# Kernel optimization log

Hardware: AMD Instinct MI355X
Metric: run time of the kernel (lower is better)

Reference implementation:

```python
import jax, jax.numpy as jnp
import numpy as np

P, B, FEAT, HID, ATTN, NHEAD = 4096, 32, 512, 512, 512, 8
HD = ATTN // NHEAD  # 64


def setup_inputs() -> dict:
    key = jax.random.key(0)
    ks = jax.random.split(key, 12)
    s = lambda n: 1.0 / np.sqrt(n)
    return {
        "last_hidden": jax.random.normal(ks[0], (1, B, HID), jnp.float32),
        "encoder_outputs": jax.random.normal(ks[1], (P, B, FEAT), jnp.float32),
        # outer projections (stored [in, out]; torch Linear is x @ W.T + b)
        "Wa_w": jax.random.uniform(ks[2], (FEAT, ATTN), jnp.float32, -s(FEAT), s(FEAT)),
        "Wa_b": jax.random.uniform(ks[3], (ATTN,), jnp.float32, -s(FEAT), s(FEAT)),
        "Ua_w": jax.random.uniform(ks[4], (HID, ATTN), jnp.float32, -s(HID), s(HID)),
        "Ua_b": jax.random.uniform(ks[5], (ATTN,), jnp.float32, -s(HID), s(HID)),
        # inner Attention(head_attn_size, head_attn_size, head_attn_size)
        "Wa2_w": jax.random.uniform(ks[6], (HD, HD), jnp.float32, -s(HD), s(HD)),
        "Wa2_b": jax.random.uniform(ks[7], (HD,), jnp.float32, -s(HD), s(HD)),
        "Ua2_w": jax.random.uniform(ks[8], (HD, HD), jnp.float32, -s(HD), s(HD)),
        "Ua2_b": jax.random.uniform(ks[9], (HD,), jnp.float32, -s(HD), s(HD)),
        "va_w": jax.random.uniform(ks[10], (HD, 1), jnp.float32, -s(HD), s(HD)),
        "va_b": jax.random.uniform(ks[11], (1,), jnp.float32, -s(HD), s(HD)),
        "nhead": NHEAD,
    }


def reference(last_hidden, encoder_outputs, Wa_w, Wa_b, Ua_w, Ua_b,
              Wa2_w, Wa2_b, Ua2_w, Ua2_b, va_w, va_b, nhead):
    p, b = encoder_outputs.shape[:2]
    enc = encoder_outputs @ Wa_w + Wa_b            # [P,B,A]
    hid = last_hidden @ Ua_w + Ua_b                # [1,B,A]
    hd = enc.shape[-1] // nhead
    enc = enc.reshape(p, b, nhead, hd)             # [P,B,nh,hd]
    hid = hid.reshape(1, b, nhead, hd)             # [1,B,nh,hd]
    # inner Bahdanau attention
    a = jnp.tanh((enc @ Wa2_w + Wa2_b) + (hid @ Ua2_w + Ua2_b))
    scores = a @ va_w + va_b                       # [P,B,nh,1]
    weights = jax.nn.softmax(scores, axis=0)       # softmax over pixels
    context = jnp.sum(weights * enc, axis=0, keepdims=True)  # [1,B,nh,hd]
    weight = jnp.mean(weights, axis=-2)            # mean over heads -> [P,B,1]
    context = context.reshape(1, b, nhead * hd)    # [1,B,A]
    return context, weight
```

## Files before the change

kernel.cpp:

```cpp
#include <hip/hip_runtime.h>
#include <hip/hip_bf16.h>

#define PDIM 4096
#define BDIM 32
#define MDIM (PDIM*BDIM)
#define KDIM 512
#define NDIM 512
#define NH   8
#define HD   64

typedef __attribute__((ext_vector_type(4))) float f32x4;
typedef __attribute__((ext_vector_type(8))) short bf16x8;

__device__ __forceinline__ unsigned short f2bf(float f) {
  unsigned u = __float_as_uint(f);
  u += 0x7fffu + ((u >> 16) & 1u);
  return (unsigned short)(u >> 16);
}
__device__ __forceinline__ float bf2f(unsigned short u) {
  return __uint_as_float(((unsigned)u) << 16);
}

__device__ __forceinline__ float fast_tanh(float x) {
  x = fminf(fmaxf(x, -15.f), 15.f);
  float e = __expf(2.f * x);
  return __fdividef(e - 1.f, e + 1.f);
}

#define GLOAD_LDS16(g, l) __builtin_amdgcn_global_load_lds( \
    (const __attribute__((address_space(1))) void*)(g),     \
    (__attribute__((address_space(3))) void*)(l), 16, 0, 0)

__global__ __launch_bounds__(256) void cvt_k(
    const float* __restrict__ x, unsigned short* __restrict__ xbf) {
  size_t i = ((size_t)blockIdx.x * 256 + threadIdx.x) * 8;
  float4 a = *(const float4*)(x + i);
  float4 b = *(const float4*)(x + i + 4);
  ushort4 o0; o0.x = f2bf(a.x); o0.y = f2bf(a.y); o0.z = f2bf(a.z); o0.w = f2bf(a.w);
  ushort4 o1; o1.x = f2bf(b.x); o1.y = f2bf(b.y); o1.z = f2bf(b.z); o1.w = f2bf(b.w);
  *(ushort4*)(xbf + i) = o0;
  *(ushort4*)(xbf + i + 4) = o1;
}

__global__ __launch_bounds__(512) void hub_k(
    const float* __restrict__ lh, const float* __restrict__ Ua,
    const float* __restrict__ Ua_b, const float* __restrict__ Ua2,
    const float* __restrict__ Ua2_b, const float* __restrict__ Wa_b,
    const float* __restrict__ Wa2, const float* __restrict__ Wa2_b,
    float* __restrict__ ubf) {
  int b = blockIdx.x, tid = threadIdx.x;
  __shared__ float ls[512];
  __shared__ float hs[512];
  ls[tid] = lh[b*512 + tid];
  __syncthreads();
  float s = Ua_b[tid];
  #pragma unroll 8
  for (int k = 0; k < 512; ++k)
    s += ls[k] * Ua[(size_t)k*512 + tid];
  hs[tid] = s;
  __syncthreads();
  int h = tid >> 6, j = tid & 63;
  float u = Ua2_b[j] + Wa2_b[j];
  #pragma unroll 4
  for (int k = 0; k < 64; ++k) {
    u += hs[h*64 + k] * Ua2[k*64 + j];
    u += Wa_b[h*64 + k] * Wa2[k*64 + j];
  }
  ubf[b*512 + tid] = u;
}

__global__ __launch_bounds__(256) void wft_k(
    const float* __restrict__ Wa, const float* __restrict__ Wa2,
    unsigned short* __restrict__ WfT) {
  int n = blockIdx.x, tid = threadIdx.x;
  int h = n >> 6, j = n & 63;
  __shared__ float w2[64];
  if (tid < 64) w2[tid] = Wa2[tid*64 + j];
  __syncthreads();
  for (int k = tid; k < 512; k += 256) {
    float s = 0.f;
    #pragma unroll 8
    for (int kk = 0; kk < 64; ++kk)
      s += Wa[(size_t)k*512 + h*64 + kk] * w2[kk];
    WfT[(size_t)n*512 + k] = f2bf(s);
  }
}

__global__ __launch_bounds__(256, 3) void gemm_score_k(
    const unsigned short* __restrict__ xbf, const unsigned short* __restrict__ WfT,
    const float* __restrict__ ubf, const float* __restrict__ va_w,
    const float* __restrict__ va_b, float* __restrict__ scores) {
  __shared__ __align__(16) unsigned short As[8192];
  __shared__ __align__(16) unsigned short Bs[8192];
  __shared__ float ubf_s[32*128];
  int tid = threadIdx.x;
  int bn = blockIdx.x, bm = blockIdx.y;
  int m0 = bm*128, n0 = bn*128;
  #pragma unroll
  for (int t = 0; t < 16; ++t) {
    int idx = t*256 + tid;
    ubf_s[idx] = ubf[(idx >> 7)*512 + n0 + (idx & 127)];
  }
  int lane = tid & 63, w = tid >> 6;
  int quad = lane >> 4, l16 = lane & 15;
  int wr = w >> 1, wc = w & 1;
  f32x4 acc[4][4] = {};

  for (int k0 = 0; k0 < KDIM; k0 += 64) {
    __syncthreads();
    #pragma unroll
    for (int i = 0; i < 4; ++i) {
      int c = i*256 + tid;
      int r = c & 127, kc = c >> 7;
      GLOAD_LDS16(xbf + (size_t)(m0 + r)*512 + k0 + kc*8, As + (size_t)c*8);
    }
    #pragma unroll
    for (int i = 0; i < 4; ++i) {
      int c = i*256 + tid;
      int r = c & 127, kc = c >> 7;
      GLOAD_LDS16(WfT + (size_t)(n0 + r)*512 + k0 + kc*8, Bs + (size_t)c*8);
    }
    __syncthreads();
    #pragma unroll
    for (int kk = 0; kk < 64; kk += 32) {
      int kc = (kk >> 3) + quad;
      bf16x8 af[4], bfr[4];
      #pragma unroll
      for (int ti = 0; ti < 4; ++ti)
        af[ti] = *(const bf16x8*)(As + ((size_t)kc*128 + 64*wr + 16*ti + l16)*8);
      #pragma unroll
      for (int tj = 0; tj < 4; ++tj)
        bfr[tj] = *(const bf16x8*)(Bs + ((size_t)kc*128 + 64*wc + 16*tj + l16)*8);
      #pragma unroll
      for (int ti = 0; ti < 4; ++ti)
        #pragma unroll
        for (int tj = 0; tj < 4; ++tj)
          acc[ti][tj] = __builtin_amdgcn_mfma_f32_16x16x32_bf16(
              af[ti], bfr[tj], acc[ti][tj], 0, 0, 0);
    }
  }

  int head = bn*2 + wc;
  float va_r[4];
  #pragma unroll
  for (int tj = 0; tj < 4; ++tj) va_r[tj] = va_w[16*tj + l16];
  float vb = va_b[0];
  #pragma unroll
  for (int ti = 0; ti < 4; ++ti) {
    #pragma unroll
    for (int r = 0; r < 4; ++r) {
      int row_loc = 64*wr + 16*ti + 4*quad + r;
      int b31 = row_loc & 31;
      float s = 0.f;
      #pragma unroll
      for (int tj = 0; tj < 4; ++tj) {
        float xa = acc[ti][tj][r] + ubf_s[b31*128 + 64*wc + 16*tj + l16];
        s += fast_tanh(xa) * va_r[tj];
      }
      s += __shfl_xor(s, 1); s += __shfl_xor(s, 2);
      s += __shfl_xor(s, 4); s += __shfl_xor(s, 8);
      if (l16 == 0) scores[(size_t)(m0 + row_loc)*NH + head] = s + vb;
    }
  }
}

__global__ __launch_bounds__(256) void softmax_k(
    const float* __restrict__ sc, float* __restrict__ w) {
  int b = blockIdx.x >> 3, h = blockIdx.x & 7;
  int tid = threadIdx.x;
  float v[16];
  float mx = -1e30f;
  #pragma unroll
  for (int i = 0; i < 16; ++i) {
    int p = tid + i*256;
    v[i] = sc[(size_t)(p*32 + b)*NH + h];
    mx = fmaxf(mx, v[i]);
  }
  for (int m = 1; m < 64; m <<= 1) mx = fmaxf(mx, __shfl_xor(mx, m));
  __shared__ float redm[4], reds[4];
  int wid = tid >> 6, lane = tid & 63;
  if (lane == 0) redm[wid] = mx;
  __syncthreads();
  mx = fmaxf(fmaxf(redm[0], redm[1]), fmaxf(redm[2], redm[3]));
  float sum = 0.f;
  #pragma unroll
  for (int i = 0; i < 16; ++i) { v[i] = __expf(v[i] - mx); sum += v[i]; }
  for (int m = 1; m < 64; m <<= 1) sum += __shfl_xor(sum, m);
  if (lane == 0) reds[wid] = sum;
  __syncthreads();
  sum = reds[0] + reds[1] + reds[2] + reds[3];
  float inv = 1.f / sum;
  #pragma unroll
  for (int i = 0; i < 16; ++i) {
    int p = tid + i*256;
    w[(size_t)(p*32 + b)*NH + h] = v[i] * inv;
  }
}

__global__ __launch_bounds__(256) void mean_k(
    const float* __restrict__ w, float* __restrict__ out) {
  int m = blockIdx.x*256 + threadIdx.x;
  const float4* p = (const float4*)(w + (size_t)m*NH);
  float4 a = p[0], c = p[1];
  out[BDIM*NDIM + m] = (a.x+a.y+a.z+a.w + c.x+c.y+c.z+c.w) * 0.125f;
}

__global__ __launch_bounds__(256) void ctx_partial_k(
    const unsigned short* __restrict__ xbf, const float* __restrict__ w,
    float* __restrict__ part) {
  int pc = blockIdx.x;
  int b  = blockIdx.y;
  int tid = threadIdx.x;
  __shared__ float wl[256*8];
  __shared__ float red[4][512];
  {
    const float4* wp = (const float4*)(w + ((size_t)((pc*256 + tid)*32 + b))*NH);
    float4 a = wp[0], c = wp[1];
    float4* dst = (float4*)(wl + tid*8);
    dst[0] = a; dst[1] = c;
  }
  __syncthreads();
  int lane = tid & 63, wv = tid >> 6;
  float acc[8][8];
  #pragma unroll
  for (int h = 0; h < 8; ++h)
    #pragma unroll
    for (int j = 0; j < 8; ++j) acc[h][j] = 0.f;
  for (int i = 0; i < 64; ++i) {
    int pl = wv*64 + i;
    bf16x8 xv = *(const bf16x8*)(xbf + ((size_t)((pc*256 + pl)*32 + b))*512 + lane*8);
    float xf[8];
    #pragma unroll
    for (int j = 0; j < 8; ++j) xf[j] = bf2f((unsigned short)xv[j]);
    #pragma unroll
    for (int h = 0; h < 8; ++h) {
      float ww = wl[pl*8 + h];
      #pragma unroll
      for (int j = 0; j < 8; ++j) acc[h][j] += ww * xf[j];
    }
  }
  for (int h = 0; h < 8; ++h) {
    #pragma unroll
    for (int j = 0; j < 8; j += 4)
      *(float4*)(&red[wv][lane*8 + j]) = *(float4*)(&acc[h][j]);
    __syncthreads();
    if (tid < 64) {
      #pragma unroll
      for (int j = 0; j < 8; ++j) {
        int f = tid*8 + j;
        part[((size_t)(b*16 + pc)*NH + h)*512 + f] =
            red[0][f] + red[1][f] + red[2][f] + red[3][f];
      }
    }
    __syncthreads();
  }
}

__global__ __launch_bounds__(256) void ctx_reduce_k(
    const float* __restrict__ part, float* __restrict__ cx) {
  int gid = blockIdx.x*256 + threadIdx.x;
  int f = gid & 511;
  int bh = gid >> 9;
  int h = bh & 7, b = bh >> 3;
  float s = 0.f;
  #pragma unroll
  for (int pc = 0; pc < 16; ++pc)
    s += part[((size_t)(b*16 + pc)*NH + h)*512 + f];
  cx[gid] = s;
}

__global__ __launch_bounds__(256) void ctx_proj_k(
    const float* __restrict__ cx, const float* __restrict__ Wa,
    const float* __restrict__ Wa_b, float* __restrict__ out) {
  int b = blockIdx.x >> 3, h = blockIdx.x & 7;
  int tid = threadIdx.x;
  __shared__ float cs[512];
  cs[tid]       = cx[(size_t)blockIdx.x*512 + tid];
  cs[tid + 256] = cx[(size_t)blockIdx.x*512 + tid + 256];
  __syncthreads();
  int d = tid & 63, g = tid >> 6;
  float s = 0.f;
  #pragma unroll 8
  for (int f = g*128; f < g*128 + 128; ++f)
    s += cs[f] * Wa[(size_t)f*512 + h*64 + d];
  __shared__ float red[256];
  red[tid] = s;
  __syncthreads();
  if (tid < 64) {
    float tot = red[tid] + red[64+tid] + red[128+tid] + red[192+tid] + Wa_b[h*64 + tid];
    out[b*512 + h*64 + tid] = tot;
  }
}

extern "C" void kernel_launch(void* const* d_in, const int* in_sizes, int n_in,
                              void* d_out, int out_size, void* d_ws, size_t ws_size,
                              hipStream_t stream) {
  (void)in_sizes; (void)n_in; (void)out_size; (void)ws_size;
  const float* lh    = (const float*)d_in[0];
  const float* x     = (const float*)d_in[1];
  const float* Wa_w  = (const float*)d_in[2];
  const float* Wa_b  = (const float*)d_in[3];
  const float* Ua_w  = (const float*)d_in[4];
  const float* Ua_b  = (const float*)d_in[5];
  const float* Wa2_w = (const float*)d_in[6];
  const float* Wa2_b = (const float*)d_in[7];
  const float* Ua2_w = (const float*)d_in[8];
  const float* Ua2_b = (const float*)d_in[9];
  const float* va_w  = (const float*)d_in[10];
  const float* va_b  = (const float*)d_in[11];
  float* out = (float*)d_out;
  char* ws = (char*)d_ws;

  unsigned short* xbf = (unsigned short*)(ws);
  unsigned short* WfT = (unsigned short*)(ws + 134217728);
  float* ubf    = (float*)(ws + 134742016);
  float* scores = (float*)(ws + 134807552);
  float* w      = (float*)(ws + 139001856);
  float* part   = (float*)(ws + 143196160);
  float* cx     = (float*)(ws + 151584768);

  hipLaunchKernelGGL(cvt_k, dim3(32768), dim3(256), 0, stream, x, xbf);
  hipLaunchKernelGGL(hub_k, dim3(32), dim3(512), 0, stream,
                     lh, Ua_w, Ua_b, Ua2_w, Ua2_b, Wa_b, Wa2_w, Wa2_b, ubf);
  hipLaunchKernelGGL(wft_k, dim3(512), dim3(256), 0, stream, Wa_w, Wa2_w, WfT);
  hipLaunchKernelGGL(gemm_score_k, dim3(4, 1024), dim3(256), 0, stream,
                     xbf, WfT, ubf, va_w, va_b, scores);
  hipLaunchKernelGGL(softmax_k, dim3(256), dim3(256), 0, stream, scores, w);
  hipLaunchKernelGGL(mean_k, dim3(512), dim3(256), 0, stream, w, out);
  hipLaunchKernelGGL(ctx_partial_k, dim3(16, 32), dim3(256), 0, stream, xbf, w, part);
  hipLaunchKernelGGL(ctx_reduce_k, dim3(512), dim3(256), 0, stream, part, cx);
  hipLaunchKernelGGL(ctx_proj_k, dim3(256), dim3(256), 0, stream, cx, Wa_w, Wa_b, out);
}
```

Measured before the change: 655.3 us.

## Store scores and weights head-major per pixel row; drop LDS ubf staging in GEMM

Scores and softmax weights are now stored as [head*32+b][P] rows, so the softmax kernel reads and writes contiguous rows instead of strided gathers. The mean and context kernels are rewritten to read this layout, with mean transposing through shared memory. The GEMM kernel stops staging the bias tile in LDS and reads it from global memory in the epilogue, freeing LDS so occupancy can rise from 3 to 4 blocks. The trade-off is GEMM stores with a stride of PDIM and uncached-pattern global bias loads in the epilogue.

```diff
diff --git a/kernel.cpp b/kernel.cpp
--- a/kernel.cpp
+++ b/kernel.cpp
@@ -86,21 +86,15 @@
   }
 }
 
-__global__ __launch_bounds__(256, 3) void gemm_score_k(
+__global__ __launch_bounds__(256, 4) void gemm_score_k(
     const unsigned short* __restrict__ xbf, const unsigned short* __restrict__ WfT,
     const float* __restrict__ ubf, const float* __restrict__ va_w,
     const float* __restrict__ va_b, float* __restrict__ scores) {
   __shared__ __align__(16) unsigned short As[8192];
   __shared__ __align__(16) unsigned short Bs[8192];
-  __shared__ float ubf_s[32*128];
   int tid = threadIdx.x;
   int bn = blockIdx.x, bm = blockIdx.y;
   int m0 = bm*128, n0 = bn*128;
-  #pragma unroll
-  for (int t = 0; t < 16; ++t) {
-    int idx = t*256 + tid;
-    ubf_s[idx] = ubf[(idx >> 7)*512 + n0 + (idx & 127)];
-  }
   int lane = tid & 63, w = tid >> 6;
   int quad = lane >> 4, l16 = lane & 15;
   int wr = w >> 1, wc = w & 1;
@@ -145,6 +139,7 @@
   #pragma unroll
   for (int tj = 0; tj < 4; ++tj) va_r[tj] = va_w[16*tj + l16];
   float vb = va_b[0];
+  const float* ubf_col = ubf + n0 + 64*wc + l16;
   #pragma unroll
   for (int ti = 0; ti < 4; ++ti) {
     #pragma unroll
@@ -154,26 +149,27 @@
       float s = 0.f;
       #pragma unroll
       for (int tj = 0; tj < 4; ++tj) {
-        float xa = acc[ti][tj][r] + ubf_s[b31*128 + 64*wc + 16*tj + l16];
+        float xa = acc[ti][tj][r] + ubf_col[b31*512 + 16*tj];
         s += fast_tanh(xa) * va_r[tj];
       }
       s += __shfl_xor(s, 1); s += __shfl_xor(s, 2);
       s += __shfl_xor(s, 4); s += __shfl_xor(s, 8);
-      if (l16 == 0) scores[(size_t)(m0 + row_loc)*NH + head] = s + vb;
+      if (l16 == 0)
+        scores[(size_t)(head*32 + b31)*PDIM + bm*4 + (row_loc >> 5)] = s + vb;
     }
   }
 }
 
 __global__ __launch_bounds__(256) void softmax_k(
     const float* __restrict__ sc, float* __restrict__ w) {
-  int b = blockIdx.x >> 3, h = blockIdx.x & 7;
-  int tid = threadIdx.x;
+  int row = blockIdx.x;
+  int tid = threadIdx.x;
+  const float* s = sc + (size_t)row*PDIM;
   float v[16];
   float mx = -1e30f;
   #pragma unroll
   for (int i = 0; i < 16; ++i) {
-    int p = tid + i*256;
-    v[i] = sc[(size_t)(p*32 + b)*NH + h];
+    v[i] = s[tid + i*256];
     mx = fmaxf(mx, v[i]);
   }
   for (int m = 1; m < 64; m <<= 1) mx = fmaxf(mx, __shfl_xor(mx, m));
@@ -191,18 +187,34 @@
   sum = reds[0] + reds[1] + reds[2] + reds[3];
   float inv = 1.f / sum;
   #pragma unroll
-  for (int i = 0; i < 16; ++i) {
-    int p = tid + i*256;
-    w[(size_t)(p*32 + b)*NH + h] = v[i] * inv;
-  }
+  for (int i = 0; i < 16; ++i)
+    w[(size_t)row*PDIM + tid + i*256] = v[i] * inv;
 }
 
 __global__ __launch_bounds__(256) void mean_k(
     const float* __restrict__ w, float* __restrict__ out) {
-  int m = blockIdx.x*256 + threadIdx.x;
-  const float4* p = (const float4*)(w + (size_t)m*NH);
-  float4 a = p[0], c = p[1];
-  out[BDIM*NDIM + m] = (a.x+a.y+a.z+a.w + c.x+c.y+c.z+c.w) * 0.125f;
+  int tid = threadIdx.x;
+  int p0 = blockIdx.x * 32;
+  int b = tid >> 3, j = tid & 7;
+  float4 s = {0.f, 0.f, 0.f, 0.f};
+  #pragma unroll
+  for (int h = 0; h < NH; ++h) {
+    float4 v = *(const float4*)(w + (size_t)(h*32 + b)*PDIM + p0 + j*4);
+    s.x += v.x; s.y += v.y; s.z += v.z; s.w += v.w;
+  }
+  __shared__ float l[32][33];
+  l[j*4+0][b] = s.x * 0.125f;
+  l[j*4+1][b] = s.y * 0.125f;
+  l[j*4+2][b] = s.z * 0.125f;
+  l[j*4+3][b] = s.w * 0.125f;
+  __syncthreads();
+  float4 o;
+  int mm = tid*4;
+  o.x = l[(mm+0) >> 5][(mm+0) & 31];
+  o.y = l[(mm+1) >> 5][(mm+1) & 31];
+  o.z = l[(mm+2) >> 5][(mm+2) & 31];
+  o.w = l[(mm+3) >> 5][(mm+3) & 31];
+  *(float4*)(out + BDIM*NDIM + (size_t)p0*32 + mm) = o;
 }
 
 __global__ __launch_bounds__(256) void ctx_partial_k(
@@ -211,13 +223,14 @@
   int pc = blockIdx.x;
   int b  = blockIdx.y;
   int tid = threadIdx.x;
-  __shared__ float wl[256*8];
+  __shared__ float wl[8*256];
   __shared__ float red[4][512];
   {
-    const float4* wp = (const float4*)(w + ((size_t)((pc*256 + tid)*32 + b))*NH);
-    float4 a = wp[0], c = wp[1];
-    float4* dst = (float4*)(wl + tid*8);
-    dst[0] = a; dst[1] = c;
+    int hq = tid >> 5, l = tid & 31;
+    const float* wrow = w + (size_t)(hq*32 + b)*PDIM + pc*256 + l*8;
+    float4 a = ((const float4*)wrow)[0], c = ((const float4*)wrow)[1];
+    float* dst = wl + hq*256 + l*8;
+    ((float4*)dst)[0] = a; ((float4*)dst)[1] = c;
   }
   __syncthreads();
   int lane = tid & 63, wv = tid >> 6;
@@ -234,7 +247,7 @@
     for (int j = 0; j < 8; ++j) xf[j] = bf2f((unsigned short)xv[j]);
     #pragma unroll
     for (int h = 0; h < 8; ++h) {
-      float ww = wl[pl*8 + h];
+      float ww = wl[h*256 + pl];
       #pragma unroll
       for (int j = 0; j < 8; ++j) acc[h][j] += ww * xf[j];
     }
@@ -326,7 +339,7 @@
   hipLaunchKernelGGL(gemm_score_k, dim3(4, 1024), dim3(256), 0, stream,
                      xbf, WfT, ubf, va_w, va_b, scores);
   hipLaunchKernelGGL(softmax_k, dim3(256), dim3(256), 0, stream, scores, w);
-  hipLaunchKernelGGL(mean_k, dim3(512), dim3(256), 0, stream, w, out);
+  hipLaunchKernelGGL(mean_k, dim3(128), dim3(256), 0, stream, w, out);
   hipLaunchKernelGGL(ctx_partial_k, dim3(16, 32), dim3(256), 0, stream, xbf, w, part);
   hipLaunchKernelGGL(ctx_reduce_k, dim3(512), dim3(256), 0, stream, part, cx);
   hipLaunchKernelGGL(ctx_proj_k, dim3(256), dim3(256), 0, stream, cx, Wa_w, Wa_b, out);
```

Measured after the change: 674.2 us. +2.9%, slower.

## Swizzle GEMM LDS tiles, drop ubf smem staging, fuse context reduce into projection

Applied to the files above, without the earlier changes.

The GEMM's LDS layout changes from k-chunk-major to row-major with an XOR swizzle on the 16-byte chunk index. This makes global loads row-contiguous and is meant to avoid LDS bank conflicts on MFMA fragment reads. The ubf shared-memory staging is removed, with the bias now read directly from global memory in the epilogue, which frees LDS so occupancy can rise to 5 blocks. The separate ctx_reduce kernel is folded into the projection kernel, saving one launch and one intermediate buffer round trip. Risks are scattered uncached global reads in the epilogue and higher register pressure under the tighter launch bound.

```diff
diff --git a/kernel.cpp b/kernel.cpp
--- a/kernel.cpp
+++ b/kernel.cpp
@@ -86,24 +86,19 @@
   }
 }
 
-__global__ __launch_bounds__(256, 3) void gemm_score_k(
+__global__ __launch_bounds__(256, 5) void gemm_score_k(
     const unsigned short* __restrict__ xbf, const unsigned short* __restrict__ WfT,
     const float* __restrict__ ubf, const float* __restrict__ va_w,
     const float* __restrict__ va_b, float* __restrict__ scores) {
   __shared__ __align__(16) unsigned short As[8192];
   __shared__ __align__(16) unsigned short Bs[8192];
-  __shared__ float ubf_s[32*128];
   int tid = threadIdx.x;
   int bn = blockIdx.x, bm = blockIdx.y;
   int m0 = bm*128, n0 = bn*128;
-  #pragma unroll
-  for (int t = 0; t < 16; ++t) {
-    int idx = t*256 + tid;
-    ubf_s[idx] = ubf[(idx >> 7)*512 + n0 + (idx & 127)];
-  }
   int lane = tid & 63, w = tid >> 6;
   int quad = lane >> 4, l16 = lane & 15;
   int wr = w >> 1, wc = w & 1;
+  int swz = (tid & 7) ^ ((tid >> 3) & 7);
   f32x4 acc[4][4] = {};
 
   for (int k0 = 0; k0 < KDIM; k0 += 64) {
@@ -111,26 +106,30 @@
     #pragma unroll
     for (int i = 0; i < 4; ++i) {
       int c = i*256 + tid;
-      int r = c & 127, kc = c >> 7;
-      GLOAD_LDS16(xbf + (size_t)(m0 + r)*512 + k0 + kc*8, As + (size_t)c*8);
+      int r = c >> 3;
+      GLOAD_LDS16(xbf + (size_t)(m0 + r)*512 + k0 + swz*8, As + (size_t)c*8);
     }
     #pragma unroll
     for (int i = 0; i < 4; ++i) {
       int c = i*256 + tid;
-      int r = c & 127, kc = c >> 7;
-      GLOAD_LDS16(WfT + (size_t)(n0 + r)*512 + k0 + kc*8, Bs + (size_t)c*8);
+      int r = c >> 3;
+      GLOAD_LDS16(WfT + (size_t)(n0 + r)*512 + k0 + swz*8, Bs + (size_t)c*8);
     }
     __syncthreads();
     #pragma unroll
     for (int kk = 0; kk < 64; kk += 32) {
-      int kc = (kk >> 3) + quad;
+      int kb = kk >> 3;
       bf16x8 af[4], bfr[4];
       #pragma unroll
-      for (int ti = 0; ti < 4; ++ti)
-        af[ti] = *(const bf16x8*)(As + ((size_t)kc*128 + 64*wr + 16*ti + l16)*8);
-      #pragma unroll
-      for (int tj = 0; tj < 4; ++tj)
-        bfr[tj] = *(const bf16x8*)(Bs + ((size_t)kc*128 + 64*wc + 16*tj + l16)*8);
+      for (int ti = 0; ti < 4; ++ti) {
+        int R = 64*wr + 16*ti + l16;
+        af[ti] = *(const bf16x8*)(As + (size_t)(R*8 + ((kb + quad) ^ (R & 7)))*8);
+      }
+      #pragma unroll
+      for (int tj = 0; tj < 4; ++tj) {
+        int R = 64*wc + 16*tj + l16;
+        bfr[tj] = *(const bf16x8*)(Bs + (size_t)(R*8 + ((kb + quad) ^ (R & 7)))*8);
+      }
       #pragma unroll
       for (int ti = 0; ti < 4; ++ti)
         #pragma unroll
@@ -145,6 +144,7 @@
   #pragma unroll
   for (int tj = 0; tj < 4; ++tj) va_r[tj] = va_w[16*tj + l16];
   float vb = va_b[0];
+  const float* ubf_col = ubf + n0 + 64*wc + l16;
   #pragma unroll
   for (int ti = 0; ti < 4; ++ti) {
     #pragma unroll
@@ -154,7 +154,7 @@
       float s = 0.f;
       #pragma unroll
       for (int tj = 0; tj < 4; ++tj) {
-        float xa = acc[ti][tj][r] + ubf_s[b31*128 + 64*wc + 16*tj + l16];
+        float xa = acc[ti][tj][r] + ubf_col[b31*512 + 16*tj];
         s += fast_tanh(xa) * va_r[tj];
       }
       s += __shfl_xor(s, 1); s += __shfl_xor(s, 2);
@@ -256,27 +256,21 @@
   }
 }
 
-__global__ __launch_bounds__(256) void ctx_reduce_k(
-    const float* __restrict__ part, float* __restrict__ cx) {
-  int gid = blockIdx.x*256 + threadIdx.x;
-  int f = gid & 511;
-  int bh = gid >> 9;
-  int h = bh & 7, b = bh >> 3;
-  float s = 0.f;
-  #pragma unroll
-  for (int pc = 0; pc < 16; ++pc)
-    s += part[((size_t)(b*16 + pc)*NH + h)*512 + f];
-  cx[gid] = s;
-}
-
-__global__ __launch_bounds__(256) void ctx_proj_k(
-    const float* __restrict__ cx, const float* __restrict__ Wa,
+__global__ __launch_bounds__(256) void ctx_projred_k(
+    const float* __restrict__ part, const float* __restrict__ Wa,
     const float* __restrict__ Wa_b, float* __restrict__ out) {
-  int b = blockIdx.x >> 3, h = blockIdx.x & 7;
+  int bh = blockIdx.x;
+  int b = bh >> 3, h = bh & 7;
   int tid = threadIdx.x;
   __shared__ float cs[512];
-  cs[tid]       = cx[(size_t)blockIdx.x*512 + tid];
-  cs[tid + 256] = cx[(size_t)blockIdx.x*512 + tid + 256];
+  float s0 = 0.f, s1 = 0.f;
+  #pragma unroll
+  for (int pc = 0; pc < 16; ++pc) {
+    const float* pp = part + ((size_t)(b*16 + pc)*NH + h)*512;
+    s0 += pp[tid];
+    s1 += pp[tid + 256];
+  }
+  cs[tid] = s0; cs[tid + 256] = s1;
   __syncthreads();
   int d = tid & 63, g = tid >> 6;
   float s = 0.f;
@@ -317,7 +311,6 @@
   float* scores = (float*)(ws + 134807552);
   float* w      = (float*)(ws + 139001856);
   float* part   = (float*)(ws + 143196160);
-  float* cx     = (float*)(ws + 151584768);
 
   hipLaunchKernelGGL(cvt_k, dim3(32768), dim3(256), 0, stream, x, xbf);
   hipLaunchKernelGGL(hub_k, dim3(32), dim3(512), 0, stream,
@@ -328,6 +321,5 @@
   hipLaunchKernelGGL(softmax_k, dim3(256), dim3(256), 0, stream, scores, w);
   hipLaunchKernelGGL(mean_k, dim3(512), dim3(256), 0, stream, w, out);
   hipLaunchKernelGGL(ctx_partial_k, dim3(16, 32), dim3(256), 0, stream, xbf, w, part);
-  hipLaunchKernelGGL(ctx_reduce_k, dim3(512), dim3(256), 0, stream, part, cx);
-  hipLaunchKernelGGL(ctx_proj_k, dim3(256), dim3(256), 0, stream, cx, Wa_w, Wa_b, out);
-}
+  hipLaunchKernelGGL(ctx_projred_k, dim3(256), dim3(256), 0, stream, part, Wa_w, Wa_b, out);
+}
```

Result: slower. 718.5 us (+9.6%).
